# Performance work log

Measured on AMD Instinct MI355X. Metric: run time of the kernel, lower is better.

The kernel has to match this reference:

```python
import jax, jax.numpy as jnp
import numpy as np


def setup_inputs() -> dict:
    key = jax.random.key(0)
    k1, k2 = jax.random.split(key)
    x = jax.random.normal(k1, (2048, 512, 7, 7), dtype=jnp.float32)   # backbone feature map [B, C, H, W]
    db = jax.random.normal(k2, (50000, 512), dtype=jnp.float32)       # gallery embeddings [N, D]
    return {"x": x, "db": db}


def reference(x, db):
    # backbone output is a 4D feature map -> global average pool over H, W
    emb = x.mean(axis=(2, 3))                      # [B, 512]; width == 512 so no pad/slice
    # torch.cdist(emb, db, p=2) via ||a||^2 - 2ab + ||b||^2 decomposition
    a2 = jnp.sum(emb * emb, axis=1, keepdims=True)         # [B, 1]
    b2 = jnp.sum(db * db, axis=1)                          # [N]
    d2 = a2 - 2.0 * (emb @ db.T) + b2[None, :]             # [B, N]
    dist = jnp.sqrt(jnp.maximum(d2, 0.0))
    min_dist = jnp.min(dist, axis=1)                       # [B]
    min_idx = jnp.argmin(dist, axis=1)                     # [B] int
    return min_dist, min_idx
```

## Files before the change

### kernel.cpp

```cpp
#include <hip/hip_runtime.h>
#include <math.h>
#include <stdint.h>

#define D      512
#define K2T    1056
#define HW     49
#define BM     128
#define BN     128
#define BK     32
#define NSWEEP 4
#define KSTEPS 33
#define TTOT   (NSWEEP * KSTEPS)

typedef __attribute__((ext_vector_type(8))) _Float16 f16x8;
typedef __attribute__((ext_vector_type(4))) float f32x4;
typedef __attribute__((address_space(3))) uint32_t lds_t;
typedef const __attribute__((address_space(1))) uint32_t glb_t;

__global__ void gap_split_kernel(const float* __restrict__ x,
                                 _Float16* __restrict__ emb2, int rows) {
    int r = blockIdx.x * blockDim.x + threadIdx.x;
    if (r >= rows) return;
    const float* p = x + (size_t)r * HW;
    float s = 0.f;
#pragma unroll
    for (int j = 0; j < HW; ++j) s += p[j];
    s *= (1.f / 49.f);
    _Float16 hi = (_Float16)s;
    _Float16 lo = (_Float16)(s - (float)hi);
    int m = r >> 9, c = r & 511;
    emb2[(size_t)m * K2T + c]       = hi;
    emb2[(size_t)m * K2T + 512 + c] = lo;
}

__global__ void finishA_kernel(_Float16* __restrict__ emb2, int M) {
    int row = blockIdx.x * 4 + (threadIdx.x >> 6);
    if (row >= M) return;
    int lane = threadIdx.x & 63;
    _Float16* p = emb2 + (size_t)row * K2T;
    f16x8 h = *(const f16x8*)(p + lane * 8);
    f16x8 l = *(const f16x8*)(p + 512 + lane * 8);
    float s = 0.f;
#pragma unroll
    for (int i = 0; i < 8; ++i) { float v = (float)h[i] + (float)l[i]; s = fmaf(v, v, s); }
#pragma unroll
    for (int m2 = 32; m2; m2 >>= 1) s += __shfl_xor(s, m2, 64);
    if (lane == 0) {
        _Float16 a2h = (_Float16)s;
        _Float16 a2l = (_Float16)(s - (float)a2h);
        _Float16 one = (_Float16)1.f, z0 = (_Float16)0.f;
        f16x8 t0 = {one, one, a2h, a2l, z0, z0, z0, z0};
        f16x8 z  = {z0, z0, z0, z0, z0, z0, z0, z0};
        *(f16x8*)(p + 1024) = t0;
        *(f16x8*)(p + 1032) = z;
        *(f16x8*)(p + 1040) = z;
        *(f16x8*)(p + 1048) = z;
    }
}

__global__ void split_db_kernel(const float* __restrict__ db,
                                _Float16* __restrict__ db2, int N, int N2) {
    int row = blockIdx.x * 4 + (threadIdx.x >> 6);
    if (row >= N2) return;
    int lane = threadIdx.x & 63;
    _Float16* q = db2 + (size_t)row * K2T;
    _Float16 z0 = (_Float16)0.f;
    f16x8 z = {z0, z0, z0, z0, z0, z0, z0, z0};
    if (row < N) {
        const float* p = db + (size_t)row * D + lane * 8;
        float4 v0 = *(const float4*)p;
        float4 v1 = *(const float4*)(p + 4);
        float vv[8] = {v0.x, v0.y, v0.z, v0.w, v1.x, v1.y, v1.z, v1.w};
        f16x8 h, l;
        float s = 0.f;
#pragma unroll
        for (int i = 0; i < 8; ++i) {
            float v = vv[i];
            s = fmaf(v, v, s);
            float wv = -2.f * v;
            _Float16 hh = (_Float16)wv;
            h[i] = hh;
            l[i] = (_Float16)(wv - (float)hh);
        }
        *(f16x8*)(q + lane * 8)       = h;
        *(f16x8*)(q + 512 + lane * 8) = l;
#pragma unroll
        for (int m2 = 32; m2; m2 >>= 1) s += __shfl_xor(s, m2, 64);
        if (lane == 0) {
            _Float16 b2h = (_Float16)s;
            _Float16 b2l = (_Float16)(s - (float)b2h);
            _Float16 one = (_Float16)1.f;
            f16x8 t0 = {b2h, b2l, one, one, z0, z0, z0, z0};
            *(f16x8*)(q + 1024) = t0;
            *(f16x8*)(q + 1032) = z;
            *(f16x8*)(q + 1040) = z;
            *(f16x8*)(q + 1048) = z;
        }
    } else {
        *(f16x8*)(q + lane * 8)       = z;
        *(f16x8*)(q + 512 + lane * 8) = z;
        if (lane < 4) *(f16x8*)(q + 1024 + lane * 8) = z;
    }
}

__global__ void init_keys_kernel(unsigned long long* __restrict__ keys, int M) {
    int b = blockIdx.x * blockDim.x + threadIdx.x;
    if (b < M) keys[b] = ~0ull;
}

__global__ __launch_bounds__(256) void dist_kernel(
        const _Float16* __restrict__ A2, const _Float16* __restrict__ B2,
        unsigned long long* __restrict__ keys, int N, int nXcdChunk)
{
    __shared__ _Float16 lds[3 * 8192];
    const int tid  = threadIdx.x;
    const int lane = tid & 63;
    const int w    = tid >> 6;
    const int wr   = w >> 1, wc = w & 1;
    const int l15  = lane & 15, lg = lane >> 4;

    const int bb   = blockIdx.x;
    const int swz  = (bb & 7) * nXcdChunk + (bb >> 3);
    const int mBase = (swz & 15) * BM;
    const long long nSuperBase = (long long)(swz >> 4) * (BN * NSWEEP);

    const int o0 = w * 1024 + lane * 16;

    auto STAGE = [&](unsigned bufByte, int tt) {
        const int k0 = (tt % KSTEPS) * BK;
        const long long nB = nSuperBase + (long long)(tt / KSTEPS) * BN;
#pragma unroll
        for (int q = 0; q < 2; ++q) {
            const int o = o0 + q * 4096;
            const int row = o >> 6, cb = o & 63;
            const char* ga = (const char*)A2 + ((size_t)(mBase + row) * K2T + k0) * 2 + cb;
            const char* gb = (const char*)B2 + ((size_t)(nB + row) * K2T + k0) * 2 + cb;
            char* la = (char*)lds + bufByte + q * 4096 + w * 1024;
            __builtin_amdgcn_global_load_lds((glb_t*)ga, (lds_t*)la, 16, 0, 0);
            __builtin_amdgcn_global_load_lds((glb_t*)gb, (lds_t*)(la + 8192), 16, 0, 0);
        }
    };

    unsigned long long key[4][4];
#pragma unroll
    for (int mF = 0; mF < 4; ++mF)
#pragma unroll
        for (int r = 0; r < 4; ++r) key[mF][r] = ~0ull;

    f32x4 acc[4][4];
#pragma unroll
    for (int mF = 0; mF < 4; ++mF)
#pragma unroll
        for (int nF = 0; nF < 4; ++nF) acc[mF][nF] = (f32x4){0.f, 0.f, 0.f, 0.f};

    STAGE(0, 0);
    STAGE(16384, 1);
    unsigned bufR = 0, bufN = 16384, bufP = 32768;

    for (int t = 0; t < TTOT; ++t) {
        if (t < TTOT - 1) asm volatile("s_waitcnt vmcnt(4)" ::: "memory");
        else              asm volatile("s_waitcnt vmcnt(0)" ::: "memory");
        __builtin_amdgcn_s_barrier();

        const _Float16* As = (const _Float16*)((const char*)lds + bufR);
        const _Float16* Bs = As + 4096;
        f16x8 af[4], bf[4];
#pragma unroll
        for (int mF = 0; mF < 4; ++mF)
            af[mF] = *(const f16x8*)(As + (wr * 64 + mF * 16 + l15) * BK + lg * 8);
#pragma unroll
        for (int nF = 0; nF < 4; ++nF)
            bf[nF] = *(const f16x8*)(Bs + (wc * 64 + nF * 16 + l15) * BK + lg * 8);

        if (t + 2 < TTOT) STAGE(bufP, t + 2);

#pragma unroll
        for (int mF = 0; mF < 4; ++mF)
#pragma unroll
            for (int nF = 0; nF < 4; ++nF)
                acc[mF][nF] = __builtin_amdgcn_mfma_f32_16x16x32_f16(
                    af[mF], bf[nF], acc[mF][nF], 0, 0, 0);

        if (t % KSTEPS == KSTEPS - 1) {
            const long long nBase = nSuperBase + (long long)(t / KSTEPS) * BN;
#pragma unroll
            for (int nF = 0; nF < 4; ++nF) {
                const long long g = nBase + wc * 64 + nF * 16 + l15;
                if (g < N) {
#pragma unroll
                    for (int mF = 0; mF < 4; ++mF)
#pragma unroll
                        for (int r = 0; r < 4; ++r) {
                            float d2 = fmaxf(acc[mF][nF][r], 0.f);
                            unsigned long long kk =
                                ((unsigned long long)__float_as_uint(d2) << 32) |
                                (unsigned long long)(unsigned)g;
                            key[mF][r] = key[mF][r] < kk ? key[mF][r] : kk;
                        }
                }
            }
#pragma unroll
            for (int mF = 0; mF < 4; ++mF)
#pragma unroll
                for (int nF = 0; nF < 4; ++nF) acc[mF][nF] = (f32x4){0.f, 0.f, 0.f, 0.f};
        }

        unsigned tmp = bufR; bufR = bufN; bufN = bufP; bufP = tmp;
    }

#pragma unroll
    for (int mF = 0; mF < 4; ++mF)
#pragma unroll
        for (int r = 0; r < 4; ++r) {
            unsigned long long k = key[mF][r];
#pragma unroll
            for (int m2 = 1; m2 < 16; m2 <<= 1) {
                unsigned long long o = __shfl_xor(k, m2, 16);
                k = k < o ? k : o;
            }
            if (l15 == 0)
                atomicMin(&keys[mBase + wr * 64 + mF * 16 + lg * 4 + r], k);
        }
}

__global__ void finalize_kernel(const unsigned long long* __restrict__ keys,
                                float* __restrict__ out_dist, float* __restrict__ out_idx, int M) {
    int b = blockIdx.x * blockDim.x + threadIdx.x;
    if (b >= M) return;
    unsigned long long k = keys[b];
    float d2 = __uint_as_float((unsigned)(k >> 32));
    out_dist[b] = sqrtf(fmaxf(d2, 0.f));
    out_idx[b]  = (float)(unsigned)(k & 0xffffffffu);
}

extern "C" void kernel_launch(void* const* d_in, const int* in_sizes, int n_in,
                              void* d_out, int out_size, void* d_ws, size_t ws_size,
                              hipStream_t stream) {
    const float* x  = (const float*)d_in[0];
    const float* db = (const float*)d_in[1];
    float* out = (float*)d_out;

    const int M  = in_sizes[0] / (D * HW);
    const int N  = in_sizes[1] / D;
    const int nTiles  = (N + BN - 1) / BN;
    const int nSupers = (nTiles + NSWEEP - 1) / NSWEEP;
    const int N2 = nSupers * NSWEEP * BN;
    const int mTiles = M / BM;
    const int nBlocks = nSupers * mTiles;
    const int nXcdChunk = nBlocks / 8;

    char* ws = (char*)d_ws;
    _Float16* emb2 = (_Float16*)ws;
    _Float16* db2  = emb2 + (size_t)M * K2T;
    unsigned long long* keys =
        (unsigned long long*)(((uintptr_t)(db2 + (size_t)N2 * K2T) + 7) & ~(uintptr_t)7);

    const int rows = M * D;
    gap_split_kernel<<<(rows + 255) / 256, 256, 0, stream>>>(x, emb2, rows);
    finishA_kernel<<<(M + 3) / 4, 256, 0, stream>>>(emb2, M);
    split_db_kernel<<<(N2 + 3) / 4, 256, 0, stream>>>(db, db2, N, N2);
    init_keys_kernel<<<(M + 255) / 256, 256, 0, stream>>>(keys, M);

    dist_kernel<<<nBlocks, 256, 0, stream>>>(emb2, db2, keys, N, nXcdChunk);

    finalize_kernel<<<(M + 255) / 256, 256, 0, stream>>>(keys, out, out + M, M);
}
```

Before: 642.5 us.

## Coalesce pooling loads through LDS, swizzle GEMM LDS tiles, raise MFMA priority

The global-average-pool kernel now has each block load its 256×49 float slab cooperatively with float4 reads into shared memory, then sums per thread from LDS. Previously each thread read its own 49-float row with strided, uncoalesced loads, and this read of the ~400 MB input is the largest memory cost. The distance GEMM applies an XOR swizzle to the 16-byte column slot on both the global-to-LDS load and the fragment reads, to cut LDS bank conflicts. It also wraps the MFMA block in s_setprio. The pooling kernel now assumes the row count is a multiple of 256 and uses about 50 KB of LDS per block, which limits occupancy.

```diff
diff --git a/kernel.cpp b/kernel.cpp
--- a/kernel.cpp
+++ b/kernel.cpp
@@ -17,17 +17,26 @@
 typedef __attribute__((address_space(3))) uint32_t lds_t;
 typedef const __attribute__((address_space(1))) uint32_t glb_t;
 
-__global__ void gap_split_kernel(const float* __restrict__ x,
-                                 _Float16* __restrict__ emb2, int rows) {
-    int r = blockIdx.x * blockDim.x + threadIdx.x;
-    if (r >= rows) return;
-    const float* p = x + (size_t)r * HW;
+__global__ __launch_bounds__(256) void gap_split_kernel(const float* __restrict__ x,
+                                                        _Float16* __restrict__ emb2) {
+    __shared__ float g[256 * HW];
+    const int tid = threadIdx.x;
+    const float4* x4 = (const float4*)x + (size_t)blockIdx.x * (256 * HW / 4);
+    float4* g4 = (float4*)g;
+#pragma unroll
+    for (int i = 0; i < 12; ++i) {
+        g4[tid + i * 256] = x4[tid + i * 256];
+    }
+    if (tid < 64) g4[tid + 3072] = x4[tid + 3072];
+    __syncthreads();
+    const float* p = g + tid * HW;
     float s = 0.f;
 #pragma unroll
     for (int j = 0; j < HW; ++j) s += p[j];
     s *= (1.f / 49.f);
     _Float16 hi = (_Float16)s;
     _Float16 lo = (_Float16)(s - (float)hi);
+    int r = blockIdx.x * 256 + tid;
     int m = r >> 9, c = r & 511;
     emb2[(size_t)m * K2T + c]       = hi;
     emb2[(size_t)m * K2T + 512 + c] = lo;
@@ -132,7 +141,9 @@
 #pragma unroll
         for (int q = 0; q < 2; ++q) {
             const int o = o0 + q * 4096;
-            const int row = o >> 6, cb = o & 63;
+            const int row = o >> 6;
+            const int slot = (o >> 4) & 3;
+            const int cb = ((slot ^ ((row >> 1) & 3)) << 4);
             const char* ga = (const char*)A2 + ((size_t)(mBase + row) * K2T + k0) * 2 + cb;
             const char* gb = (const char*)B2 + ((size_t)(nB + row) * K2T + k0) * 2 + cb;
             char* la = (char*)lds + bufByte + q * 4096 + w * 1024;
@@ -157,6 +168,8 @@
     STAGE(16384, 1);
     unsigned bufR = 0, bufN = 16384, bufP = 32768;
 
+    const int sw = (lg ^ ((l15 >> 1) & 3)) * 8;
+
     for (int t = 0; t < TTOT; ++t) {
         if (t < TTOT - 1) asm volatile("s_waitcnt vmcnt(4)" ::: "memory");
         else              asm volatile("s_waitcnt vmcnt(0)" ::: "memory");
@@ -167,19 +180,21 @@
         f16x8 af[4], bf[4];
 #pragma unroll
         for (int mF = 0; mF < 4; ++mF)
-            af[mF] = *(const f16x8*)(As + (wr * 64 + mF * 16 + l15) * BK + lg * 8);
+            af[mF] = *(const f16x8*)(As + (wr * 64 + mF * 16 + l15) * BK + sw);
 #pragma unroll
         for (int nF = 0; nF < 4; ++nF)
-            bf[nF] = *(const f16x8*)(Bs + (wc * 64 + nF * 16 + l15) * BK + lg * 8);
+            bf[nF] = *(const f16x8*)(Bs + (wc * 64 + nF * 16 + l15) * BK + sw);
 
         if (t + 2 < TTOT) STAGE(bufP, t + 2);
 
+        __builtin_amdgcn_s_setprio(1);
 #pragma unroll
         for (int mF = 0; mF < 4; ++mF)
 #pragma unroll
             for (int nF = 0; nF < 4; ++nF)
                 acc[mF][nF] = __builtin_amdgcn_mfma_f32_16x16x32_f16(
                     af[mF], bf[nF], acc[mF][nF], 0, 0, 0);
+        __builtin_amdgcn_s_setprio(0);
 
         if (t % KSTEPS == KSTEPS - 1) {
             const long long nBase = nSuperBase + (long long)(t / KSTEPS) * BN;
@@ -256,7 +271,7 @@
         (unsigned long long*)(((uintptr_t)(db2 + (size_t)N2 * K2T) + 7) & ~(uintptr_t)7);
 
     const int rows = M * D;
-    gap_split_kernel<<<(rows + 255) / 256, 256, 0, stream>>>(x, emb2, rows);
+    gap_split_kernel<<<rows / 256, 256, 0, stream>>>(x, emb2);
     finishA_kernel<<<(M + 3) / 4, 256, 0, stream>>>(emb2, M);
     split_db_kernel<<<(N2 + 3) / 4, 256, 0, stream>>>(db, db2, N, N2);
     init_keys_kernel<<<(M + 255) / 256, 256, 0, stream>>>(keys, M);
```

After: 657.4 us. +2.3%, slower.
